# Optimization experiments

Hardware: AMD Instinct MI355X
Metric: run time of the kernel (lower is better)

The kernel has to match this reference:

```python
import jax, jax.numpy as jnp
import numpy as np

N_NODES = 64
N_EDGES = N_NODES * (N_NODES - 1)  # 4032 (fully connected, no self-loops)
BATCH = 64
N_IN = 64
N_HID = 128
N_OUT = 16


def _linear_params(key, fan_in, fan_out):
    # mimic torch nn.Linear default init: U(-1/sqrt(fan_in), 1/sqrt(fan_in))
    kw, kb = jax.random.split(key)
    s = 1.0 / np.sqrt(fan_in)
    W = jax.random.uniform(kw, (fan_in, fan_out), minval=-s, maxval=s, dtype=jnp.float32)
    b = jax.random.uniform(kb, (fan_out,), minval=-s, maxval=s, dtype=jnp.float32)
    return W, b


def setup_inputs() -> dict:
    key = jax.random.key(0)
    ks = jax.random.split(key, 10)
    # one-hot relation matrices for fully-connected graph without self loops
    pairs = np.array([(i, j) for i in range(N_NODES) for j in range(N_NODES) if i != j])
    eye = np.eye(N_NODES, dtype=np.float32)
    rel_send = jnp.asarray(eye[pairs[:, 0]])  # [E, N]
    rel_rec = jnp.asarray(eye[pairs[:, 1]])   # [E, N]

    x = jax.random.normal(ks[0], (BATCH, N_NODES, N_IN), dtype=jnp.float32)

    w1a, b1a = _linear_params(ks[1], N_IN, N_HID)
    w1b, b1b = _linear_params(ks[2], N_HID, N_HID)
    w2a, b2a = _linear_params(ks[3], 2 * N_HID, N_HID)
    w2b, b2b = _linear_params(ks[4], N_HID, N_HID)
    w3a, b3a = _linear_params(ks[5], N_HID, N_HID)
    w3b, b3b = _linear_params(ks[6], N_HID, N_HID)
    w4a, b4a = _linear_params(ks[7], 3 * N_HID, N_HID)  # factor=True
    w4b, b4b = _linear_params(ks[8], N_HID, N_HID)
    wout, bout = _linear_params(ks[9], N_HID, N_OUT)

    return dict(x=x, rel_rec=rel_rec, rel_send=rel_send,
                w1a=w1a, b1a=b1a, w1b=w1b, b1b=b1b,
                w2a=w2a, b2a=b2a, w2b=w2b, b2b=b2b,
                w3a=w3a, b3a=b3a, w3b=w3b, b3b=b3b,
                w4a=w4a, b4a=b4a, w4b=w4b, b4b=b4b,
                wout=wout, bout=bout)


def _mlp(x, wa, ba, wb, bb):
    # Linear -> ReLU -> Linear
    return jax.nn.relu(x @ wa + ba) @ wb + bb


def reference(x, rel_rec, rel_send,
              w1a, b1a, w1b, b1b,
              w2a, b2a, w2b, b2b,
              w3a, b3a, w3b, b3b,
              w4a, b4a, w4b, b4b,
              wout, bout):
    def node2edge(h):
        receivers = jnp.einsum('en,bnh->beh', rel_rec, h)
        senders = jnp.einsum('en,bnh->beh', rel_send, h)
        return jnp.concatenate([senders, receivers], axis=-1)  # [B,E,2H]

    def edge2node(e):
        agg = jnp.einsum('en,beh->bnh', rel_rec, e)
        norm = rel_rec.sum(0)[None, :, None]  # [1,N,1]
        return agg / (norm + 1e-6)

    h = _mlp(x, w1a, b1a, w1b, b1b)            # [B,N,H]
    e = _mlp(node2edge(h), w2a, b2a, w2b, b2b)  # [B,E,H]
    x_skip = e
    # factor=True branch
    n = _mlp(edge2node(e), w3a, b3a, w3b, b3b)  # [B,N,H]
    e2 = node2edge(n)                           # [B,E,2H]
    e2 = jnp.concatenate([e2, x_skip], axis=2)  # [B,E,3H]
    e2 = _mlp(e2, w4a, b4a, w4b, b4b)           # [B,E,H]
    return e2 @ wout + bout                     # [B,E,n_out]
```

## Files before the change

### kernel.cpp

```cpp
#include <hip/hip_runtime.h>
#include <hip/hip_bf16.h>


#define DI __device__ __forceinline__

typedef short bf16x8 __attribute__((ext_vector_type(8)));
typedef float f32x4 __attribute__((ext_vector_type(4)));
typedef unsigned short u16;

static constexpr int NN = 64, NE = 4032, H = 128;

DI u16 f2bf(float f) {
  union { float f; unsigned u; } v; v.f = f;
  unsigned u = v.u;
  return (u16)((u + 0x7fffu + ((u >> 16) & 1u)) >> 16);
}
DI unsigned pk2(float a, float b) {
  union { __hip_bfloat162 h; unsigned u; } c;
  c.h = __float22bfloat162_rn(float2{a, b});
  return c.u;
}
DI f32x4 mf(bf16x8 a, bf16x8 b, f32x4 c) {
  return __builtin_amdgcn_mfma_f32_16x16x32_bf16(a, b, c, 0, 0, 0);
}
DI bf16x8 ldfrag(const u16* __restrict__ p, int idx, int l) {
  return *reinterpret_cast<const bf16x8*>(p + (idx * 64 + l) * 8);
}

__global__ __launch_bounds__(64) void prepack_kernel(
    const float* __restrict__ w1a, const float* __restrict__ w1b,
    const float* __restrict__ w2a, const float* __restrict__ w2b,
    const float* __restrict__ w3a, const float* __restrict__ w3b,
    const float* __restrict__ w4a, const float* __restrict__ w4b,
    const float* __restrict__ wout,
    const float* __restrict__ b2b, const float* __restrict__ b4b,
    const float* __restrict__ bout,
    u16* __restrict__ pk, float* __restrict__ c2, float* __restrict__ c4) {
  int seg = blockIdx.y, f = blockIdx.x, l = threadIdx.x;
  int h = l >> 4, mm = l & 15;
  if (seg == 10) {
    if (f >= 4) return;
    union { u16 u[8]; uint4 q; } o;
#pragma unroll
    for (int jj = 0; jj < 8; jj++) {
      int row = f * 32 + h * 8 + jj;
      float s = 0.f;
      for (int j = 0; j < 128; j++) s += w4b[row * 128 + j] * wout[j * 16 + mm];
      o.u[jj] = f2bf(s);
    }
    *reinterpret_cast<uint4*>(pk + ((304 + f) * 64 + l) * 8) = o.q;
    return;
  }
  if (seg == 11) {
    if (f < 2) {
      int o = f * 64 + l;
      float s = 0.f;
      for (int k = 0; k < 128; k++) s += b2b[k] * w4a[(256 + k) * 128 + o];
      c2[o] = s;
    } else if (f == 2 && l < 16) {
      float s = bout[l];
      for (int k = 0; k < 128; k++) s += b4b[k] * wout[k * 16 + l];
      c4[l] = s;
    }
    return;
  }
  const float* src; int foff, nfrag, roff, pi;
  switch (seg) {
    case 0:  src = w1a; foff = 0;   nfrag = 16; roff = 0;   pi = 0; break;
    case 1:  src = w1b; foff = 16;  nfrag = 32; roff = 0;   pi = 1; break;
    case 2:  src = w2a; foff = 48;  nfrag = 32; roff = 0;   pi = 1; break;
    case 3:  src = w2a; foff = 80;  nfrag = 32; roff = 128; pi = 1; break;
    case 4:  src = w2b; foff = 112; nfrag = 32; roff = 0;   pi = 0; break;
    case 5:  src = w3a; foff = 144; nfrag = 32; roff = 0;   pi = 1; break;
    case 6:  src = w3b; foff = 176; nfrag = 32; roff = 0;   pi = 1; break;
    case 7:  src = w4a; foff = 208; nfrag = 32; roff = 0;   pi = 1; break;
    case 8:  src = w4a; foff = 240; nfrag = 32; roff = 128; pi = 1; break;
    default: src = w4a; foff = 272; nfrag = 32; roff = 256; pi = 0; break;
  }
  if (f >= nfrag) return;
  int kt = f >> 3, ct = f & 7;
  union { u16 u[8]; uint4 q; } o;
#pragma unroll
  for (int jj = 0; jj < 8; jj++) {
    int row = pi ? (kt * 32 + (jj >> 2) * 16 + h * 4 + (jj & 3))
                 : (kt * 32 + h * 8 + jj);
    o.u[jj] = f2bf(src[(roff + row) * 128 + ct * 16 + mm]);
  }
  *reinterpret_cast<uint4*>(pk + ((foff + f) * 64 + l) * 8) = o.q;
}

__global__ __launch_bounds__(256, 4) void node_kernel(
    const float* __restrict__ x, const u16* __restrict__ pk,
    const float* __restrict__ b1a, const float* __restrict__ b1b,
    const float* __restrict__ b2a,
    float* __restrict__ sproj, float* __restrict__ rproj) {
  __shared__ bf16x8 act[2][4][64];
  int blk = blockIdx.x, b = blk >> 2, nq = blk & 3;
  int tid = threadIdx.x, l = tid & 63, w = tid >> 6;
  int m = l & 15, h = l >> 4;
  int node = nq * 16 + m;
  const f32x4 Z = {0.f, 0.f, 0.f, 0.f};
  f32x4 acc0, acc1;
  {
    const float* xb = x + (b * NN + node) * 64;
    bf16x8 xin[2];
#pragma unroll
    for (int kt = 0; kt < 2; kt++) {
      f32x4 a0 = *(const f32x4*)(xb + kt * 32 + h * 8);
      f32x4 a1 = *(const f32x4*)(xb + kt * 32 + h * 8 + 4);
      union { unsigned u[4]; bf16x8 v; } t;
      t.u[0] = pk2(a0[0], a0[1]); t.u[1] = pk2(a0[2], a0[3]);
      t.u[2] = pk2(a1[0], a1[1]); t.u[3] = pk2(a1[2], a1[3]);
      xin[kt] = t.v;
    }
#pragma unroll
    for (int kt = 0; kt < 2; kt++) {
      acc0 = mf(ldfrag(pk, kt * 8 + 2 * w, l),     xin[kt], kt == 0 ? Z : acc0);
      acc1 = mf(ldfrag(pk, kt * 8 + 2 * w + 1, l), xin[kt], kt == 0 ? Z : acc1);
    }
    f32x4 bA = *(const f32x4*)(b1a + (2 * w) * 16 + h * 4);
    f32x4 bB = *(const f32x4*)(b1a + (2 * w + 1) * 16 + h * 4);
    union { unsigned u[4]; bf16x8 v; } t;
    t.u[0] = pk2(fmaxf(acc0[0] + bA[0], 0.f), fmaxf(acc0[1] + bA[1], 0.f));
    t.u[1] = pk2(fmaxf(acc0[2] + bA[2], 0.f), fmaxf(acc0[3] + bA[3], 0.f));
    t.u[2] = pk2(fmaxf(acc1[0] + bB[0], 0.f), fmaxf(acc1[1] + bB[1], 0.f));
    t.u[3] = pk2(fmaxf(acc1[2] + bB[2], 0.f), fmaxf(acc1[3] + bB[3], 0.f));
    act[0][w][l] = t.v;
  }
  __syncthreads();
  bf16x8 ef[4];
#pragma unroll
  for (int kt = 0; kt < 4; kt++) ef[kt] = act[0][kt][l];
#pragma unroll
  for (int kt = 0; kt < 4; kt++) {
    acc0 = mf(ldfrag(pk + 16 * 512, kt * 8 + 2 * w, l),     ef[kt], kt == 0 ? Z : acc0);
    acc1 = mf(ldfrag(pk + 16 * 512, kt * 8 + 2 * w + 1, l), ef[kt], kt == 0 ? Z : acc1);
  }
  {
    f32x4 bA = *(const f32x4*)(b1b + (2 * w) * 16 + h * 4);
    f32x4 bB = *(const f32x4*)(b1b + (2 * w + 1) * 16 + h * 4);
    union { unsigned u[4]; bf16x8 v; } t;
    t.u[0] = pk2(acc0[0] + bA[0], acc0[1] + bA[1]);
    t.u[1] = pk2(acc0[2] + bA[2], acc0[3] + bA[3]);
    t.u[2] = pk2(acc1[0] + bB[0], acc1[1] + bB[1]);
    t.u[3] = pk2(acc1[2] + bB[2], acc1[3] + bB[3]);
    act[1][w][l] = t.v;
  }
  __syncthreads();
#pragma unroll
  for (int kt = 0; kt < 4; kt++) ef[kt] = act[1][kt][l];
#pragma unroll
  for (int kt = 0; kt < 4; kt++) {
    acc0 = mf(ldfrag(pk + 48 * 512, kt * 8 + 2 * w, l),     ef[kt], kt == 0 ? Z : acc0);
    acc1 = mf(ldfrag(pk + 48 * 512, kt * 8 + 2 * w + 1, l), ef[kt], kt == 0 ? Z : acc1);
  }
  float* spo = sproj + (b * NN + node) * H;
  *reinterpret_cast<f32x4*>(spo + (2 * w) * 16 + h * 4) = acc0;
  *reinterpret_cast<f32x4*>(spo + (2 * w + 1) * 16 + h * 4) = acc1;
#pragma unroll
  for (int kt = 0; kt < 4; kt++) {
    acc0 = mf(ldfrag(pk + 80 * 512, kt * 8 + 2 * w, l),     ef[kt], kt == 0 ? Z : acc0);
    acc1 = mf(ldfrag(pk + 80 * 512, kt * 8 + 2 * w + 1, l), ef[kt], kt == 0 ? Z : acc1);
  }
  {
    f32x4 bA = *(const f32x4*)(b2a + (2 * w) * 16 + h * 4);
    f32x4 bB = *(const f32x4*)(b2a + (2 * w + 1) * 16 + h * 4);
    float* rpo = rproj + (b * NN + node) * H;
    f32x4 o0 = acc0, o1 = acc1;
    o0[0] += bA[0]; o0[1] += bA[1]; o0[2] += bA[2]; o0[3] += bA[3];
    o1[0] += bB[0]; o1[1] += bB[1]; o1[2] += bB[2]; o1[3] += bB[3];
    *reinterpret_cast<f32x4*>(rpo + (2 * w) * 16 + h * 4) = o0;
    *reinterpret_cast<f32x4*>(rpo + (2 * w + 1) * 16 + h * 4) = o1;
  }
}

__global__ __launch_bounds__(256, 3) void agg_kernel(
    const float* __restrict__ sproj, const float* __restrict__ rproj,
    const u16* __restrict__ pk,
    const float* __restrict__ b2b, const float* __restrict__ b3a,
    const float* __restrict__ b3b, const float* __restrict__ b4a,
    const float* __restrict__ c2,
    float* __restrict__ s4, float* __restrict__ r4) {
  __shared__ f32x4 lred[4][8][64];
  __shared__ bf16x8 act[2][4][64];
  int blk = blockIdx.x, b = blk >> 2, jq = blk & 3;
  int tid = threadIdx.x, l = tid & 63, w = tid >> 6, m = l & 15, h = l >> 4;
  int j = jq * 16 + m;
  const float* rpb = rproj + (b * NN + j) * H;
  f32x4 rpv[8], accS[8];
#pragma unroll
  for (int k = 0; k < 8; k++) {
    rpv[k] = *(const f32x4*)(rpb + (k >> 1) * 32 + h * 8 + (k & 1) * 4);
    accS[k] = f32x4{0.f, 0.f, 0.f, 0.f};
  }
  const float* spb = sproj + b * NN * H;
  for (int i = w * 16; i < w * 16 + 16; i++) {
    const float* sp = spb + i * H;
#pragma unroll
    for (int k = 0; k < 8; k++) {
      f32x4 s = *(const f32x4*)(sp + (k >> 1) * 32 + h * 8 + (k & 1) * 4);
      f32x4 t = s + rpv[k];
      t[0] = fmaxf(t[0], 0.f); t[1] = fmaxf(t[1], 0.f);
      t[2] = fmaxf(t[2], 0.f); t[3] = fmaxf(t[3], 0.f);
      accS[k] += t;
    }
  }
  if (w == jq) {
    const float* sp = spb + j * H;
#pragma unroll
    for (int k = 0; k < 8; k++) {
      f32x4 s = *(const f32x4*)(sp + (k >> 1) * 32 + h * 8 + (k & 1) * 4);
      f32x4 t = s + rpv[k];
      accS[k][0] -= fmaxf(t[0], 0.f); accS[k][1] -= fmaxf(t[1], 0.f);
      accS[k][2] -= fmaxf(t[2], 0.f); accS[k][3] -= fmaxf(t[3], 0.f);
    }
  }
#pragma unroll
  for (int k = 0; k < 8; k++) lred[w][k][l] = accS[k];
  __syncthreads();
  {
    f32x4 s0 = lred[0][2 * w][l] + lred[1][2 * w][l] + lred[2][2 * w][l] + lred[3][2 * w][l];
    f32x4 s1 = lred[0][2 * w + 1][l] + lred[1][2 * w + 1][l] + lred[2][2 * w + 1][l] + lred[3][2 * w + 1][l];
    union { unsigned u[4]; bf16x8 v; } t;
    t.u[0] = pk2(s0[0], s0[1]); t.u[1] = pk2(s0[2], s0[3]);
    t.u[2] = pk2(s1[0], s1[1]); t.u[3] = pk2(s1[2], s1[3]);
    act[0][w][l] = t.v;
  }
  __syncthreads();
  const f32x4 Z = {0.f, 0.f, 0.f, 0.f};
  f32x4 acc0, acc1;
  bf16x8 ef[4];
#pragma unroll
  for (int kt = 0; kt < 4; kt++) ef[kt] = act[0][kt][l];
#pragma unroll
  for (int kt = 0; kt < 4; kt++) {
    acc0 = mf(ldfrag(pk + 112 * 512, kt * 8 + 2 * w, l),     ef[kt], kt == 0 ? Z : acc0);
    acc1 = mf(ldfrag(pk + 112 * 512, kt * 8 + 2 * w + 1, l), ef[kt], kt == 0 ? Z : acc1);
  }
  {
    const float inv = 1.0f / (63.0f + 1e-6f);
    const float binv = 63.0f * inv;
    f32x4 bA = *(const f32x4*)(b2b + (2 * w) * 16 + h * 4);
    f32x4 bB = *(const f32x4*)(b2b + (2 * w + 1) * 16 + h * 4);
    union { unsigned u[4]; bf16x8 v; } t;
    t.u[0] = pk2(acc0[0] * inv + bA[0] * binv, acc0[1] * inv + bA[1] * binv);
    t.u[1] = pk2(acc0[2] * inv + bA[2] * binv, acc0[3] * inv + bA[3] * binv);
    t.u[2] = pk2(acc1[0] * inv + bB[0] * binv, acc1[1] * inv + bB[1] * binv);
    t.u[3] = pk2(acc1[2] * inv + bB[2] * binv, acc1[3] * inv + bB[3] * binv);
    act[1][w][l] = t.v;
  }
  __syncthreads();
#pragma unroll
  for (int kt = 0; kt < 4; kt++) ef[kt] = act[1][kt][l];
#pragma unroll
  for (int kt = 0; kt < 4; kt++) {
    acc0 = mf(ldfrag(pk + 144 * 512, kt * 8 + 2 * w, l),     ef[kt], kt == 0 ? Z : acc0);
    acc1 = mf(ldfrag(pk + 144 * 512, kt * 8 + 2 * w + 1, l), ef[kt], kt == 0 ? Z : acc1);
  }
  {
    f32x4 bA = *(const f32x4*)(b3a + (2 * w) * 16 + h * 4);
    f32x4 bB = *(const f32x4*)(b3a + (2 * w + 1) * 16 + h * 4);
    union { unsigned u[4]; bf16x8 v; } t;
    t.u[0] = pk2(fmaxf(acc0[0] + bA[0], 0.f), fmaxf(acc0[1] + bA[1], 0.f));
    t.u[1] = pk2(fmaxf(acc0[2] + bA[2], 0.f), fmaxf(acc0[3] + bA[3], 0.f));
    t.u[2] = pk2(fmaxf(acc1[0] + bB[0], 0.f), fmaxf(acc1[1] + bB[1], 0.f));
    t.u[3] = pk2(fmaxf(acc1[2] + bB[2], 0.f), fmaxf(acc1[3] + bB[3], 0.f));
    act[0][w][l] = t.v;
  }
  __syncthreads();
#pragma unroll
  for (int kt = 0; kt < 4; kt++) ef[kt] = act[0][kt][l];
#pragma unroll
  for (int kt = 0; kt < 4; kt++) {
    acc0 = mf(ldfrag(pk + 176 * 512, kt * 8 + 2 * w, l),     ef[kt], kt == 0 ? Z : acc0);
    acc1 = mf(ldfrag(pk + 176 * 512, kt * 8 + 2 * w + 1, l), ef[kt], kt == 0 ? Z : acc1);
  }
  {
    f32x4 bA = *(const f32x4*)(b3b + (2 * w) * 16 + h * 4);
    f32x4 bB = *(const f32x4*)(b3b + (2 * w + 1) * 16 + h * 4);
    union { unsigned u[4]; bf16x8 v; } t;
    t.u[0] = pk2(acc0[0] + bA[0], acc0[1] + bA[1]);
    t.u[1] = pk2(acc0[2] + bA[2], acc0[3] + bA[3]);
    t.u[2] = pk2(acc1[0] + bB[0], acc1[1] + bB[1]);
    t.u[3] = pk2(acc1[2] + bB[2], acc1[3] + bB[3]);
    act[1][w][l] = t.v;
  }
  __syncthreads();
#pragma unroll
  for (int kt = 0; kt < 4; kt++) ef[kt] = act[1][kt][l];
#pragma unroll
  for (int kt = 0; kt < 4; kt++) {
    acc0 = mf(ldfrag(pk + 208 * 512, kt * 8 + 2 * w, l),     ef[kt], kt == 0 ? Z : acc0);
    acc1 = mf(ldfrag(pk + 208 * 512, kt * 8 + 2 * w + 1, l), ef[kt], kt == 0 ? Z : acc1);
  }
  {
    f32x4 cA = *(const f32x4*)(c2 + (2 * w) * 16 + h * 4);
    f32x4 cB = *(const f32x4*)(c2 + (2 * w + 1) * 16 + h * 4);
    float* s4o = s4 + (b * NN + j) * H;
    f32x4 o0 = acc0, o1 = acc1;
    o0[0] += cA[0]; o0[1] += cA[1]; o0[2] += cA[2]; o0[3] += cA[3];
    o1[0] += cB[0]; o1[1] += cB[1]; o1[2] += cB[2]; o1[3] += cB[3];
    *reinterpret_cast<f32x4*>(s4o + (2 * w) * 16 + h * 4) = o0;
    *reinterpret_cast<f32x4*>(s4o + (2 * w + 1) * 16 + h * 4) = o1;
  }
#pragma unroll
  for (int kt = 0; kt < 4; kt++) {
    acc0 = mf(ldfrag(pk + 240 * 512, kt * 8 + 2 * w, l),     ef[kt], kt == 0 ? Z : acc0);
    acc1 = mf(ldfrag(pk + 240 * 512, kt * 8 + 2 * w + 1, l), ef[kt], kt == 0 ? Z : acc1);
  }
  {
    f32x4 bA = *(const f32x4*)(b4a + (2 * w) * 16 + h * 4);
    f32x4 bB = *(const f32x4*)(b4a + (2 * w + 1) * 16 + h * 4);
    float* r4o = r4 + (b * NN + j) * H;
    f32x4 o0 = acc0, o1 = acc1;
    o0[0] += bA[0]; o0[1] += bA[1]; o0[2] += bA[2]; o0[3] += bA[3];
    o1[0] += bB[0]; o1[1] += bB[1]; o1[2] += bB[2]; o1[3] += bB[3];
    *reinterpret_cast<f32x4*>(r4o + (2 * w) * 16 + h * 4) = o0;
    *reinterpret_cast<f32x4*>(r4o + (2 * w + 1) * 16 + h * 4) = o1;
  }
}

__global__ __launch_bounds__(256, 4) void edge_kernel(
    const float* __restrict__ sproj, const float* __restrict__ rproj,
    const float* __restrict__ s4, const float* __restrict__ r4,
    const u16* __restrict__ pk, const float* __restrict__ c4,
    float* __restrict__ out) {
  __shared__ alignas(16) u16 bufA[8192];
  __shared__ alignas(16) u16 bufB[8192];
  int blk = blockIdx.x;
  int b = blk >> 6, i = blk & 63;
  int tid = threadIdx.x, l = tid & 63, w = tid >> 6;
  int m16 = l & 15, h = l >> 4;
  const f32x4 Z = {0.f, 0.f, 0.f, 0.f};
  int jnv[4];
#pragma unroll
  for (int n = 0; n < 4; n++) {
    int e = n * 16 + m16;
    int v = e + (e >= i ? 1 : 0); jnv[n] = v > 63 ? 63 : v;
  }
  {
    const float* spp = sproj + (b * NN + i) * H + w * 32 + h * 8;
    f32x4 s0 = *(const f32x4*)spp, s1 = *(const f32x4*)(spp + 4);
#pragma unroll
    for (int n = 0; n < 4; n++) {
      const float* rpp = rproj + (b * NN + jnv[n]) * H + w * 32 + h * 8;
      f32x4 r0 = *(const f32x4*)rpp, r1 = *(const f32x4*)(rpp + 4);
      union { unsigned u[4]; uint4 q; } t;
      t.u[0] = pk2(fmaxf(s0[0] + r0[0], 0.f), fmaxf(s0[1] + r0[1], 0.f));
      t.u[1] = pk2(fmaxf(s0[2] + r0[2], 0.f), fmaxf(s0[3] + r0[3], 0.f));
      t.u[2] = pk2(fmaxf(s1[0] + r1[0], 0.f), fmaxf(s1[1] + r1[1], 0.f));
      t.u[3] = pk2(fmaxf(s1[2] + r1[2], 0.f), fmaxf(s1[3] + r1[3], 0.f));
      *reinterpret_cast<uint4*>(&bufA[((w * 4 + n) * 64 + l) * 8]) = t.q;
    }
  }
  bf16x8 wv[8];
#pragma unroll
  for (int idx = 0; idx < 8; idx++)
    wv[idx] = ldfrag(pk + 112 * 512, (idx >> 1) * 8 + 2 * w + (idx & 1), l);
  __syncthreads();
  f32x4 acc[2][4];
#pragma unroll
  for (int n = 0; n < 4; n++) {
    bf16x8 bf[4];
#pragma unroll
    for (int kt = 0; kt < 4; kt++)
      bf[kt] = *reinterpret_cast<const bf16x8*>(&bufA[((kt * 4 + n) * 64 + l) * 8]);
#pragma unroll
    for (int kt = 0; kt < 4; kt++)
#pragma unroll
      for (int m = 0; m < 2; m++)
        acc[m][n] = mf(wv[kt * 2 + m], bf[kt], kt == 0 ? Z : acc[m][n]);
  }
#pragma unroll
  for (int idx = 0; idx < 8; idx++)
    wv[idx] = ldfrag(pk + 272 * 512, (idx >> 1) * 8 + 2 * w + (idx & 1), l);
  {
    int lane2b = (h >> 1) * 16 + m16;
    int jb = (h & 1) * 4;
#pragma unroll
    for (int m = 0; m < 2; m++)
#pragma unroll
      for (int n = 0; n < 4; n++) {
        union { unsigned u[2]; unsigned long long d; } p;
        p.u[0] = pk2(acc[m][n][0], acc[m][n][1]);
        p.u[1] = pk2(acc[m][n][2], acc[m][n][3]);
        *reinterpret_cast<unsigned long long*>(
            &bufB[((w * 4 + n) * 64 + lane2b + m * 32) * 8 + jb]) = p.d;
      }
  }
  __syncthreads();
#pragma unroll
  for (int n = 0; n < 4; n++) {
    bf16x8 bf[4];
#pragma unroll
    for (int kt = 0; kt < 4; kt++)
      bf[kt] = *reinterpret_cast<const bf16x8*>(&bufB[((kt * 4 + n) * 64 + l) * 8]);
#pragma unroll
    for (int kt = 0; kt < 4; kt++)
#pragma unroll
      for (int m = 0; m < 2; m++)
        acc[m][n] = mf(wv[kt * 2 + m], bf[kt], kt == 0 ? Z : acc[m][n]);
  }
  {
    f32x4 s4v[2];
#pragma unroll
    for (int m = 0; m < 2; m++)
      s4v[m] = *(const f32x4*)(s4 + (b * NN + i) * H + w * 32 + m * 16 + h * 4);
    int lane2b = (h >> 1) * 16 + m16;
    int jb = (h & 1) * 4;
#pragma unroll
    for (int n = 0; n < 4; n++) {
      const float* r4p = r4 + (b * NN + jnv[n]) * H + w * 32 + h * 4;
#pragma unroll
      for (int m = 0; m < 2; m++) {
        f32x4 rv = *(const f32x4*)(r4p + m * 16);
        union { unsigned u[2]; unsigned long long d; } p;
        p.u[0] = pk2(fmaxf(acc[m][n][0] + s4v[m][0] + rv[0], 0.f),
                     fmaxf(acc[m][n][1] + s4v[m][1] + rv[1], 0.f));
        p.u[1] = pk2(fmaxf(acc[m][n][2] + s4v[m][2] + rv[2], 0.f),
                     fmaxf(acc[m][n][3] + s4v[m][3] + rv[3], 0.f));
        *reinterpret_cast<unsigned long long*>(
            &bufA[((w * 4 + n) * 64 + lane2b + m * 32) * 8 + jb]) = p.d;
      }
    }
  }
  __syncthreads();
  {
    bf16x8 wfv[4], bf[4];
#pragma unroll
    for (int kt = 0; kt < 4; kt++) {
      wfv[kt] = ldfrag(pk + 304 * 512, kt, l);
      bf[kt] = *reinterpret_cast<const bf16x8*>(&bufA[((kt * 4 + w) * 64 + l) * 8]);
    }
    f32x4 a4 = Z;
#pragma unroll
    for (int kt = 0; kt < 4; kt++) a4 = mf(wfv[kt], bf[kt], a4);
    int jj = w * 16 + m16;
    if (jj < 63) {
      f32x4 c4v = *(const f32x4*)(c4 + h * 4);
      f32x4 o;
      o[0] = a4[0] + c4v[0]; o[1] = a4[1] + c4v[1];
      o[2] = a4[2] + c4v[2]; o[3] = a4[3] + c4v[3];
      *reinterpret_cast<f32x4*>(out + (b * NE + i * 63 + jj) * 16 + h * 4) = o;
    }
  }
}

extern "C" void kernel_launch(void* const* d_in, const int* in_sizes, int n_in,
                              void* d_out, int out_size, void* d_ws, size_t ws_size,
                              hipStream_t stream) {
  const float* x    = (const float*)d_in[0];
  const float* w1a  = (const float*)d_in[3];
  const float* b1a  = (const float*)d_in[4];
  const float* w1b  = (const float*)d_in[5];
  const float* b1b  = (const float*)d_in[6];
  const float* w2a  = (const float*)d_in[7];
  const float* b2a  = (const float*)d_in[8];
  const float* w2b  = (const float*)d_in[9];
  const float* b2b  = (const float*)d_in[10];
  const float* w3a  = (const float*)d_in[11];
  const float* b3a  = (const float*)d_in[12];
  const float* w3b  = (const float*)d_in[13];
  const float* b3b  = (const float*)d_in[14];
  const float* w4a  = (const float*)d_in[15];
  const float* b4a  = (const float*)d_in[16];
  const float* w4b  = (const float*)d_in[17];
  const float* b4b  = (const float*)d_in[18];
  const float* wout = (const float*)d_in[19];
  const float* bout = (const float*)d_in[20];
  float* out = (float*)d_out;

  float* sproj = (float*)d_ws;
  float* rproj = sproj + 524288;
  float* s4    = rproj + 524288;
  float* r4    = s4 + 524288;
  u16* pkw     = (u16*)(r4 + 524288);
  float* c2    = (float*)(pkw + 174080);
  float* c4    = c2 + 128;

  prepack_kernel<<<dim3(32, 12), 64, 0, stream>>>(
      w1a, w1b, w2a, w2b, w3a, w3b, w4a, w4b, wout, b2b, b4b, bout, pkw, c2, c4);
  node_kernel<<<256, 256, 0, stream>>>(x, pkw, b1a, b1b, b2a, sproj, rproj);
  agg_kernel<<<256, 256, 0, stream>>>(sproj, rproj, pkw, b2b, b3a, b3b, b4a, c2, s4, r4);
  edge_kernel<<<4096, 256, 0, stream>>>(sproj, rproj, s4, r4, pkw, c4, out);
}
```

Baseline: 94.25 us.

## Widen node/agg kernels to 8 waves, prefetch edge epilogue loads, add setprio

The node and aggregation kernels move from 4 waves with two output tiles each to 8 waves with one tile each. The agg reduction is split across 8 waves with a larger LDS reduction buffer. The edge kernel gets a remapped block index to interleave batches, and it prefetches the s4/r4 epilogue loads before the barrier. It also raises wave priority around the MFMA loops. The prepack dot products use multiple accumulators to break dependency chains. Together these aim to raise parallelism and hide latency, at the cost of more LDS and register pressure and extra barrier participants.

```diff
diff --git a/kernel.cpp b/kernel.cpp
--- a/kernel.cpp
+++ b/kernel.cpp
@@ -7,6 +7,7 @@
 typedef short bf16x8 __attribute__((ext_vector_type(8)));
 typedef float f32x4 __attribute__((ext_vector_type(4)));
 typedef unsigned short u16;
+typedef unsigned long long u64;
 
 static constexpr int NN = 64, NE = 4032, H = 128;
 
@@ -44,9 +45,14 @@
 #pragma unroll
     for (int jj = 0; jj < 8; jj++) {
       int row = f * 32 + h * 8 + jj;
-      float s = 0.f;
-      for (int j = 0; j < 128; j++) s += w4b[row * 128 + j] * wout[j * 16 + mm];
-      o.u[jj] = f2bf(s);
+      float s0 = 0.f, s1 = 0.f, s2 = 0.f, s3 = 0.f;
+      for (int j = 0; j < 128; j += 4) {
+        s0 += w4b[row * 128 + j]     * wout[j * 16 + mm];
+        s1 += w4b[row * 128 + j + 1] * wout[(j + 1) * 16 + mm];
+        s2 += w4b[row * 128 + j + 2] * wout[(j + 2) * 16 + mm];
+        s3 += w4b[row * 128 + j + 3] * wout[(j + 3) * 16 + mm];
+      }
+      o.u[jj] = f2bf((s0 + s1) + (s2 + s3));
     }
     *reinterpret_cast<uint4*>(pk + ((304 + f) * 64 + l) * 8) = o.q;
     return;
@@ -54,9 +60,12 @@
   if (seg == 11) {
     if (f < 2) {
       int o = f * 64 + l;
-      float s = 0.f;
-      for (int k = 0; k < 128; k++) s += b2b[k] * w4a[(256 + k) * 128 + o];
-      c2[o] = s;
+      float s0 = 0.f, s1 = 0.f;
+      for (int k = 0; k < 128; k += 2) {
+        s0 += b2b[k] * w4a[(256 + k) * 128 + o];
+        s1 += b2b[k + 1] * w4a[(256 + k + 1) * 128 + o];
+      }
+      c2[o] = s0 + s1;
     } else if (f == 2 && l < 16) {
       float s = bout[l];
       for (int k = 0; k < 128; k++) s += b4b[k] * wout[k * 16 + l];
@@ -89,7 +98,7 @@
   *reinterpret_cast<uint4*>(pk + ((foff + f) * 64 + l) * 8) = o.q;
 }
 
-__global__ __launch_bounds__(256, 4) void node_kernel(
+__global__ __launch_bounds__(512, 2) void node_kernel(
     const float* __restrict__ x, const u16* __restrict__ pk,
     const float* __restrict__ b1a, const float* __restrict__ b1b,
     const float* __restrict__ b2a,
@@ -100,7 +109,7 @@
   int m = l & 15, h = l >> 4;
   int node = nq * 16 + m;
   const f32x4 Z = {0.f, 0.f, 0.f, 0.f};
-  f32x4 acc0, acc1;
+  f32x4 acc;
   {
     const float* xb = x + (b * NN + node) * 64;
     bf16x8 xin[2];
@@ -113,75 +122,54 @@
       t.u[2] = pk2(a1[0], a1[1]); t.u[3] = pk2(a1[2], a1[3]);
       xin[kt] = t.v;
     }
-#pragma unroll
-    for (int kt = 0; kt < 2; kt++) {
-      acc0 = mf(ldfrag(pk, kt * 8 + 2 * w, l),     xin[kt], kt == 0 ? Z : acc0);
-      acc1 = mf(ldfrag(pk, kt * 8 + 2 * w + 1, l), xin[kt], kt == 0 ? Z : acc1);
-    }
-    f32x4 bA = *(const f32x4*)(b1a + (2 * w) * 16 + h * 4);
-    f32x4 bB = *(const f32x4*)(b1a + (2 * w + 1) * 16 + h * 4);
-    union { unsigned u[4]; bf16x8 v; } t;
-    t.u[0] = pk2(fmaxf(acc0[0] + bA[0], 0.f), fmaxf(acc0[1] + bA[1], 0.f));
-    t.u[1] = pk2(fmaxf(acc0[2] + bA[2], 0.f), fmaxf(acc0[3] + bA[3], 0.f));
-    t.u[2] = pk2(fmaxf(acc1[0] + bB[0], 0.f), fmaxf(acc1[1] + bB[1], 0.f));
-    t.u[3] = pk2(fmaxf(acc1[2] + bB[2], 0.f), fmaxf(acc1[3] + bB[3], 0.f));
-    act[0][w][l] = t.v;
+    acc = mf(ldfrag(pk, w, l), xin[0], Z);
+    acc = mf(ldfrag(pk, 8 + w, l), xin[1], acc);
+    f32x4 bb = *(const f32x4*)(b1a + w * 16 + h * 4);
+    union { unsigned u[2]; u64 d; } p;
+    p.u[0] = pk2(fmaxf(acc[0] + bb[0], 0.f), fmaxf(acc[1] + bb[1], 0.f));
+    p.u[1] = pk2(fmaxf(acc[2] + bb[2], 0.f), fmaxf(acc[3] + bb[3], 0.f));
+    reinterpret_cast<u64*>(&act[0][w >> 1][l])[w & 1] = p.d;
   }
   __syncthreads();
   bf16x8 ef[4];
 #pragma unroll
   for (int kt = 0; kt < 4; kt++) ef[kt] = act[0][kt][l];
 #pragma unroll
-  for (int kt = 0; kt < 4; kt++) {
-    acc0 = mf(ldfrag(pk + 16 * 512, kt * 8 + 2 * w, l),     ef[kt], kt == 0 ? Z : acc0);
-    acc1 = mf(ldfrag(pk + 16 * 512, kt * 8 + 2 * w + 1, l), ef[kt], kt == 0 ? Z : acc1);
-  }
-  {
-    f32x4 bA = *(const f32x4*)(b1b + (2 * w) * 16 + h * 4);
-    f32x4 bB = *(const f32x4*)(b1b + (2 * w + 1) * 16 + h * 4);
-    union { unsigned u[4]; bf16x8 v; } t;
-    t.u[0] = pk2(acc0[0] + bA[0], acc0[1] + bA[1]);
-    t.u[1] = pk2(acc0[2] + bA[2], acc0[3] + bA[3]);
-    t.u[2] = pk2(acc1[0] + bB[0], acc1[1] + bB[1]);
-    t.u[3] = pk2(acc1[2] + bB[2], acc1[3] + bB[3]);
-    act[1][w][l] = t.v;
+  for (int kt = 0; kt < 4; kt++)
+    acc = mf(ldfrag(pk + 16 * 512, kt * 8 + w, l), ef[kt], kt == 0 ? Z : acc);
+  {
+    f32x4 bb = *(const f32x4*)(b1b + w * 16 + h * 4);
+    union { unsigned u[2]; u64 d; } p;
+    p.u[0] = pk2(acc[0] + bb[0], acc[1] + bb[1]);
+    p.u[1] = pk2(acc[2] + bb[2], acc[3] + bb[3]);
+    reinterpret_cast<u64*>(&act[1][w >> 1][l])[w & 1] = p.d;
   }
   __syncthreads();
 #pragma unroll
   for (int kt = 0; kt < 4; kt++) ef[kt] = act[1][kt][l];
 #pragma unroll
-  for (int kt = 0; kt < 4; kt++) {
-    acc0 = mf(ldfrag(pk + 48 * 512, kt * 8 + 2 * w, l),     ef[kt], kt == 0 ? Z : acc0);
-    acc1 = mf(ldfrag(pk + 48 * 512, kt * 8 + 2 * w + 1, l), ef[kt], kt == 0 ? Z : acc1);
-  }
-  float* spo = sproj + (b * NN + node) * H;
-  *reinterpret_cast<f32x4*>(spo + (2 * w) * 16 + h * 4) = acc0;
-  *reinterpret_cast<f32x4*>(spo + (2 * w + 1) * 16 + h * 4) = acc1;
-#pragma unroll
-  for (int kt = 0; kt < 4; kt++) {
-    acc0 = mf(ldfrag(pk + 80 * 512, kt * 8 + 2 * w, l),     ef[kt], kt == 0 ? Z : acc0);
-    acc1 = mf(ldfrag(pk + 80 * 512, kt * 8 + 2 * w + 1, l), ef[kt], kt == 0 ? Z : acc1);
-  }
-  {
-    f32x4 bA = *(const f32x4*)(b2a + (2 * w) * 16 + h * 4);
-    f32x4 bB = *(const f32x4*)(b2a + (2 * w + 1) * 16 + h * 4);
-    float* rpo = rproj + (b * NN + node) * H;
-    f32x4 o0 = acc0, o1 = acc1;
-    o0[0] += bA[0]; o0[1] += bA[1]; o0[2] += bA[2]; o0[3] += bA[3];
-    o1[0] += bB[0]; o1[1] += bB[1]; o1[2] += bB[2]; o1[3] += bB[3];
-    *reinterpret_cast<f32x4*>(rpo + (2 * w) * 16 + h * 4) = o0;
-    *reinterpret_cast<f32x4*>(rpo + (2 * w + 1) * 16 + h * 4) = o1;
-  }
-}
-
-__global__ __launch_bounds__(256, 3) void agg_kernel(
+  for (int kt = 0; kt < 4; kt++)
+    acc = mf(ldfrag(pk + 48 * 512, kt * 8 + w, l), ef[kt], kt == 0 ? Z : acc);
+  *reinterpret_cast<f32x4*>(sproj + (b * NN + node) * H + w * 16 + h * 4) = acc;
+#pragma unroll
+  for (int kt = 0; kt < 4; kt++)
+    acc = mf(ldfrag(pk + 80 * 512, kt * 8 + w, l), ef[kt], kt == 0 ? Z : acc);
+  {
+    f32x4 bb = *(const f32x4*)(b2a + w * 16 + h * 4);
+    f32x4 o = acc;
+    o[0] += bb[0]; o[1] += bb[1]; o[2] += bb[2]; o[3] += bb[3];
+    *reinterpret_cast<f32x4*>(rproj + (b * NN + node) * H + w * 16 + h * 4) = o;
+  }
+}
+
+__global__ __launch_bounds__(512, 2) void agg_kernel(
     const float* __restrict__ sproj, const float* __restrict__ rproj,
     const u16* __restrict__ pk,
     const float* __restrict__ b2b, const float* __restrict__ b3a,
     const float* __restrict__ b3b, const float* __restrict__ b4a,
     const float* __restrict__ c2,
     float* __restrict__ s4, float* __restrict__ r4) {
-  __shared__ f32x4 lred[4][8][64];
+  __shared__ f32x4 lred[8][8][64];
   __shared__ bf16x8 act[2][4][64];
   int blk = blockIdx.x, b = blk >> 2, jq = blk & 3;
   int tid = threadIdx.x, l = tid & 63, w = tid >> 6, m = l & 15, h = l >> 4;
@@ -194,7 +182,7 @@
     accS[k] = f32x4{0.f, 0.f, 0.f, 0.f};
   }
   const float* spb = sproj + b * NN * H;
-  for (int i = w * 16; i < w * 16 + 16; i++) {
+  for (int i = w * 8; i < w * 8 + 8; i++) {
     const float* sp = spb + i * H;
 #pragma unroll
     for (int k = 0; k < 8; k++) {
@@ -205,7 +193,7 @@
       accS[k] += t;
     }
   }
-  if (w == jq) {
+  if ((j >> 3) == w) {
     const float* sp = spb + j * H;
 #pragma unroll
     for (int k = 0; k < 8; k++) {
@@ -218,9 +206,13 @@
 #pragma unroll
   for (int k = 0; k < 8; k++) lred[w][k][l] = accS[k];
   __syncthreads();
-  {
-    f32x4 s0 = lred[0][2 * w][l] + lred[1][2 * w][l] + lred[2][2 * w][l] + lred[3][2 * w][l];
-    f32x4 s1 = lred[0][2 * w + 1][l] + lred[1][2 * w + 1][l] + lred[2][2 * w + 1][l] + lred[3][2 * w + 1][l];
+  if (w < 4) {
+    f32x4 s0 = f32x4{0.f, 0.f, 0.f, 0.f}, s1 = s0;
+#pragma unroll
+    for (int ww = 0; ww < 8; ww++) {
+      s0 += lred[ww][2 * w][l];
+      s1 += lred[ww][2 * w + 1][l];
+    }
     union { unsigned u[4]; bf16x8 v; } t;
     t.u[0] = pk2(s0[0], s0[1]); t.u[1] = pk2(s0[2], s0[3]);
     t.u[2] = pk2(s1[0], s1[1]); t.u[3] = pk2(s1[2], s1[3]);
@@ -228,95 +220,68 @@
   }
   __syncthreads();
   const f32x4 Z = {0.f, 0.f, 0.f, 0.f};
-  f32x4 acc0, acc1;
+  f32x4 acc;
   bf16x8 ef[4];
 #pragma unroll
   for (int kt = 0; kt < 4; kt++) ef[kt] = act[0][kt][l];
 #pragma unroll
-  for (int kt = 0; kt < 4; kt++) {
-    acc0 = mf(ldfrag(pk + 112 * 512, kt * 8 + 2 * w, l),     ef[kt], kt == 0 ? Z : acc0);
-    acc1 = mf(ldfrag(pk + 112 * 512, kt * 8 + 2 * w + 1, l), ef[kt], kt == 0 ? Z : acc1);
-  }
+  for (int kt = 0; kt < 4; kt++)
+    acc = mf(ldfrag(pk + 112 * 512, kt * 8 + w, l), ef[kt], kt == 0 ? Z : acc);
   {
     const float inv = 1.0f / (63.0f + 1e-6f);
     const float binv = 63.0f * inv;
-    f32x4 bA = *(const f32x4*)(b2b + (2 * w) * 16 + h * 4);
-    f32x4 bB = *(const f32x4*)(b2b + (2 * w + 1) * 16 + h * 4);
-    union { unsigned u[4]; bf16x8 v; } t;
-    t.u[0] = pk2(acc0[0] * inv + bA[0] * binv, acc0[1] * inv + bA[1] * binv);
-    t.u[1] = pk2(acc0[2] * inv + bA[2] * binv, acc0[3] * inv + bA[3] * binv);
-    t.u[2] = pk2(acc1[0] * inv + bB[0] * binv, acc1[1] * inv + bB[1] * binv);
-    t.u[3] = pk2(acc1[2] * inv + bB[2] * binv, acc1[3] * inv + bB[3] * binv);
-    act[1][w][l] = t.v;
+    f32x4 bb = *(const f32x4*)(b2b + w * 16 + h * 4);
+    union { unsigned u[2]; u64 d; } p;
+    p.u[0] = pk2(acc[0] * inv + bb[0] * binv, acc[1] * inv + bb[1] * binv);
+    p.u[1] = pk2(acc[2] * inv + bb[2] * binv, acc[3] * inv + bb[3] * binv);
+    reinterpret_cast<u64*>(&act[1][w >> 1][l])[w & 1] = p.d;
   }
   __syncthreads();
 #pragma unroll
   for (int kt = 0; kt < 4; kt++) ef[kt] = act[1][kt][l];
 #pragma unroll
-  for (int kt = 0; kt < 4; kt++) {
-    acc0 = mf(ldfrag(pk + 144 * 512, kt * 8 + 2 * w, l),     ef[kt], kt == 0 ? Z : acc0);
-    acc1 = mf(ldfrag(pk + 144 * 512, kt * 8 + 2 * w + 1, l), ef[kt], kt == 0 ? Z : acc1);
-  }
-  {
-    f32x4 bA = *(const f32x4*)(b3a + (2 * w) * 16 + h * 4);
-    f32x4 bB = *(const f32x4*)(b3a + (2 * w + 1) * 16 + h * 4);
-    union { unsigned u[4]; bf16x8 v; } t;
-    t.u[0] = pk2(fmaxf(acc0[0] + bA[0], 0.f), fmaxf(acc0[1] + bA[1], 0.f));
-    t.u[1] = pk2(fmaxf(acc0[2] + bA[2], 0.f), fmaxf(acc0[3] + bA[3], 0.f));
-    t.u[2] = pk2(fmaxf(acc1[0] + bB[0], 0.f), fmaxf(acc1[1] + bB[1], 0.f));
-    t.u[3] = pk2(fmaxf(acc1[2] + bB[2], 0.f), fmaxf(acc1[3] + bB[3], 0.f));
-    act[0][w][l] = t.v;
+  for (int kt = 0; kt < 4; kt++)
+    acc = mf(ldfrag(pk + 144 * 512, kt * 8 + w, l), ef[kt], kt == 0 ? Z : acc);
+  {
+    f32x4 bb = *(const f32x4*)(b3a + w * 16 + h * 4);
+    union { unsigned u[2]; u64 d; } p;
+    p.u[0] = pk2(fmaxf(acc[0] + bb[0], 0.f), fmaxf(acc[1] + bb[1], 0.f));
+    p.u[1] = pk2(fmaxf(acc[2] + bb[2], 0.f), fmaxf(acc[3] + bb[3], 0.f));
+    reinterpret_cast<u64*>(&act[0][w >> 1][l])[w & 1] = p.d;
   }
   __syncthreads();
 #pragma unroll
   for (int kt = 0; kt < 4; kt++) ef[kt] = act[0][kt][l];
 #pragma unroll
-  for (int kt = 0; kt < 4; kt++) {
-    acc0 = mf(ldfrag(pk + 176 * 512, kt * 8 + 2 * w, l),     ef[kt], kt == 0 ? Z : acc0);
-    acc1 = mf(ldfrag(pk + 176 * 512, kt * 8 + 2 * w + 1, l), ef[kt], kt == 0 ? Z : acc1);
-  }
-  {
-    f32x4 bA = *(const f32x4*)(b3b + (2 * w) * 16 + h * 4);
-    f32x4 bB = *(const f32x4*)(b3b + (2 * w + 1) * 16 + h * 4);
-    union { unsigned u[4]; bf16x8 v; } t;
-    t.u[0] = pk2(acc0[0] + bA[0], acc0[1] + bA[1]);
-    t.u[1] = pk2(acc0[2] + bA[2], acc0[3] + bA[3]);
-    t.u[2] = pk2(acc1[0] + bB[0], acc1[1] + bB[1]);
-    t.u[3] = pk2(acc1[2] + bB[2], acc1[3] + bB[3]);
-    act[1][w][l] = t.v;
+  for (int kt = 0; kt < 4; kt++)
+    acc = mf(ldfrag(pk + 176 * 512, kt * 8 + w, l), ef[kt], kt == 0 ? Z : acc);
+  {
+    f32x4 bb = *(const f32x4*)(b3b + w * 16 + h * 4);
+    union { unsigned u[2]; u64 d; } p;
+    p.u[0] = pk2(acc[0] + bb[0], acc[1] + bb[1]);
+    p.u[1] = pk2(acc[2] + bb[2], acc[3] + bb[3]);
+    reinterpret_cast<u64*>(&act[1][w >> 1][l])[w & 1] = p.d;
   }
   __syncthreads();
 #pragma unroll
   for (int kt = 0; kt < 4; kt++) ef[kt] = act[1][kt][l];
 #pragma unroll
-  for (int kt = 0; kt < 4; kt++) {
-    acc0 = mf(ldfrag(pk + 208 * 512, kt * 8 + 2 * w, l),     ef[kt], kt == 0 ? Z : acc0);
-    acc1 = mf(ldfrag(pk + 208 * 512, kt * 8 + 2 * w + 1, l), ef[kt], kt == 0 ? Z : acc1);
-  }
-  {
-    f32x4 cA = *(const f32x4*)(c2 + (2 * w) * 16 + h * 4);
-    f32x4 cB = *(const f32x4*)(c2 + (2 * w + 1) * 16 + h * 4);
-    float* s4o = s4 + (b * NN + j) * H;
-    f32x4 o0 = acc0, o1 = acc1;
-    o0[0] += cA[0]; o0[1] += cA[1]; o0[2] += cA[2]; o0[3] += cA[3];
-    o1[0] += cB[0]; o1[1] += cB[1]; o1[2] += cB[2]; o1[3] += cB[3];
-    *reinterpret_cast<f32x4*>(s4o + (2 * w) * 16 + h * 4) = o0;
-    *reinterpret_cast<f32x4*>(s4o + (2 * w + 1) * 16 + h * 4) = o1;
-  }
-#pragma unroll
-  for (int kt = 0; kt < 4; kt++) {
-    acc0 = mf(ldfrag(pk + 240 * 512, kt * 8 + 2 * w, l),     ef[kt], kt == 0 ? Z : acc0);
-    acc1 = mf(ldfrag(pk + 240 * 512, kt * 8 + 2 * w + 1, l), ef[kt], kt == 0 ? Z : acc1);
-  }
-  {
-    f32x4 bA = *(const f32x4*)(b4a + (2 * w) * 16 + h * 4);
-    f32x4 bB = *(const f32x4*)(b4a + (2 * w + 1) * 16 + h * 4);
-    float* r4o = r4 + (b * NN + j) * H;
-    f32x4 o0 = acc0, o1 = acc1;
-    o0[0] += bA[0]; o0[1] += bA[1]; o0[2] += bA[2]; o0[3] += bA[3];
-    o1[0] += bB[0]; o1[1] += bB[1]; o1[2] += bB[2]; o1[3] += bB[3];
-    *reinterpret_cast<f32x4*>(r4o + (2 * w) * 16 + h * 4) = o0;
-    *reinterpret_cast<f32x4*>(r4o + (2 * w + 1) * 16 + h * 4) = o1;
+  for (int kt = 0; kt < 4; kt++)
+    acc = mf(ldfrag(pk + 208 * 512, kt * 8 + w, l), ef[kt], kt == 0 ? Z : acc);
+  {
+    f32x4 cc = *(const f32x4*)(c2 + w * 16 + h * 4);
+    f32x4 o = acc;
+    o[0] += cc[0]; o[1] += cc[1]; o[2] += cc[2]; o[3] += cc[3];
+    *reinterpret_cast<f32x4*>(s4 + (b * NN + j) * H + w * 16 + h * 4) = o;
+  }
+#pragma unroll
+  for (int kt = 0; kt < 4; kt++)
+    acc = mf(ldfrag(pk + 240 * 512, kt * 8 + w, l), ef[kt], kt == 0 ? Z : acc);
+  {
+    f32x4 bb = *(const f32x4*)(b4a + w * 16 + h * 4);
+    f32x4 o = acc;
+    o[0] += bb[0]; o[1] += bb[1]; o[2] += bb[2]; o[3] += bb[3];
+    *reinterpret_cast<f32x4*>(r4 + (b * NN + j) * H + w * 16 + h * 4) = o;
   }
 }
 
@@ -328,7 +293,8 @@
   __shared__ alignas(16) u16 bufA[8192];
   __shared__ alignas(16) u16 bufB[8192];
   int blk = blockIdx.x;
-  int b = blk >> 6, i = blk & 63;
+  int wg = (blk & 7) * 512 + (blk >> 3);
+  int b = wg >> 6, i = wg & 63;
   int tid = threadIdx.x, l = tid & 63, w = tid >> 6;
   int m16 = l & 15, h = l >> 4;
   const f32x4 Z = {0.f, 0.f, 0.f, 0.f};
@@ -359,6 +325,7 @@
     wv[idx] = ldfrag(pk + 112 * 512, (idx >> 1) * 8 + 2 * w + (idx & 1), l);
   __syncthreads();
   f32x4 acc[2][4];
+  __builtin_amdgcn_s_setprio(1);
 #pragma unroll
   for (int n = 0; n < 4; n++) {
     bf16x8 bf[4];
@@ -371,6 +338,7 @@
       for (int m = 0; m < 2; m++)
         acc[m][n] = mf(wv[kt * 2 + m], bf[kt], kt == 0 ? Z : acc[m][n]);
   }
+  __builtin_amdgcn_s_setprio(0);
 #pragma unroll
   for (int idx = 0; idx < 8; idx++)
     wv[idx] = ldfrag(pk + 272 * 512, (idx >> 1) * 8 + 2 * w + (idx & 1), l);
@@ -381,14 +349,25 @@
     for (int m = 0; m < 2; m++)
 #pragma unroll
       for (int n = 0; n < 4; n++) {
-        union { unsigned u[2]; unsigned long long d; } p;
+        union { unsigned u[2]; u64 d; } p;
         p.u[0] = pk2(acc[m][n][0], acc[m][n][1]);
         p.u[1] = pk2(acc[m][n][2], acc[m][n][3]);
-        *reinterpret_cast<unsigned long long*>(
+        *reinterpret_cast<u64*>(
             &bufB[((w * 4 + n) * 64 + lane2b + m * 32) * 8 + jb]) = p.d;
       }
   }
-  __syncthreads();
+  f32x4 s4v[2], rv[4][2];
+#pragma unroll
+  for (int m = 0; m < 2; m++)
+    s4v[m] = *(const f32x4*)(s4 + (b * NN + i) * H + w * 32 + m * 16 + h * 4);
+#pragma unroll
+  for (int n = 0; n < 4; n++) {
+    const float* r4p = r4 + (b * NN + jnv[n]) * H + w * 32 + h * 4;
+#pragma unroll
+    for (int m = 0; m < 2; m++) rv[n][m] = *(const f32x4*)(r4p + m * 16);
+  }
+  __syncthreads();
+  __builtin_amdgcn_s_setprio(1);
 #pragma unroll
   for (int n = 0; n < 4; n++) {
     bf16x8 bf[4];
@@ -401,28 +380,23 @@
       for (int m = 0; m < 2; m++)
         acc[m][n] = mf(wv[kt * 2 + m], bf[kt], kt == 0 ? Z : acc[m][n]);
   }
-  {
-    f32x4 s4v[2];
-#pragma unroll
-    for (int m = 0; m < 2; m++)
-      s4v[m] = *(const f32x4*)(s4 + (b * NN + i) * H + w * 32 + m * 16 + h * 4);
+  __builtin_amdgcn_s_setprio(0);
+  {
     int lane2b = (h >> 1) * 16 + m16;
     int jb = (h & 1) * 4;
 #pragma unroll
-    for (int n = 0; n < 4; n++) {
-      const float* r4p = r4 + (b * NN + jnv[n]) * H + w * 32 + h * 4;
+    for (int n = 0; n < 4; n++)
 #pragma unroll
       for (int m = 0; m < 2; m++) {
-        f32x4 rv = *(const f32x4*)(r4p + m * 16);
-        union { unsigned u[2]; unsigned long long d; } p;
-        p.u[0] = pk2(fmaxf(acc[m][n][0] + s4v[m][0] + rv[0], 0.f),
-                     fmaxf(acc[m][n][1] + s4v[m][1] + rv[1], 0.f));
-        p.u[1] = pk2(fmaxf(acc[m][n][2] + s4v[m][2] + rv[2], 0.f),
-                     fmaxf(acc[m][n][3] + s4v[m][3] + rv[3], 0.f));
-        *reinterpret_cast<unsigned long long*>(
+        f32x4 r = rv[n][m];
+        union { unsigned u[2]; u64 d; } p;
+        p.u[0] = pk2(fmaxf(acc[m][n][0] + s4v[m][0] + r[0], 0.f),
+                     fmaxf(acc[m][n][1] + s4v[m][1] + r[1], 0.f));
+        p.u[1] = pk2(fmaxf(acc[m][n][2] + s4v[m][2] + r[2], 0.f),
+                     fmaxf(acc[m][n][3] + s4v[m][3] + r[3], 0.f));
+        *reinterpret_cast<u64*>(
             &bufA[((w * 4 + n) * 64 + lane2b + m * 32) * 8 + jb]) = p.d;
       }
-    }
   }
   __syncthreads();
   {
@@ -480,7 +454,7 @@
 
   prepack_kernel<<<dim3(32, 12), 64, 0, stream>>>(
       w1a, w1b, w2a, w2b, w3a, w3b, w4a, w4b, wout, b2b, b4b, bout, pkw, c2, c4);
-  node_kernel<<<256, 256, 0, stream>>>(x, pkw, b1a, b1b, b2a, sproj, rproj);
-  agg_kernel<<<256, 256, 0, stream>>>(sproj, rproj, pkw, b2b, b3a, b3b, b4a, c2, s4, r4);
+  node_kernel<<<256, 512, 0, stream>>>(x, pkw, b1a, b1b, b2a, sproj, rproj);
+  agg_kernel<<<256, 512, 0, stream>>>(sproj, rproj, pkw, b2b, b3a, b3b, b4a, c2, s4, r4);
   edge_kernel<<<4096, 256, 0, stream>>>(sproj, rproj, s4, r4, pkw, c4, out);
 }
```

Measured after the change: 84.68 us. 1.11x faster.
